# Performance work log

Measured on AMD Instinct MI355X. Metric: run time of the kernel, lower is better.

The kernel has to match this reference:

```python
import jax, jax.numpy as jnp
import numpy as np

KH, KW, PAD, G = 3, 3, 1, 4  # kernel, padding, deformable groups


def _bilinear_gather(xg, py, px):
    """xg: [B,G,C,Hin,Win]; py,px: [B,G,K,H,W] sample coords.
    Returns [B,G,C,K,H,W] with zero padding outside the image (mmcv semantics)."""
    B, Gd, C, Hin, Win = xg.shape
    y0 = jnp.floor(py)
    x0 = jnp.floor(px)
    wy1 = py - y0
    wx1 = px - x0
    wy0 = 1.0 - wy1
    wx0 = 1.0 - wx1
    xf = xg.reshape(B, Gd, C, Hin * Win)

    def gather(yi, xi):
        valid = (yi >= 0) & (yi < Hin) & (xi >= 0) & (xi < Win)
        yc = jnp.clip(yi, 0, Hin - 1).astype(jnp.int32)
        xc = jnp.clip(xi, 0, Win - 1).astype(jnp.int32)
        lin = (yc * Win + xc).reshape(B, Gd, 1, -1)  # [B,G,1,K*H*W]
        v = jnp.take_along_axis(xf, lin, axis=3).reshape(B, Gd, C, *yi.shape[2:])
        return v * valid[:, :, None].astype(xg.dtype)

    return (gather(y0, x0) * (wy0 * wx0)[:, :, None]
            + gather(y0, x0 + 1) * (wy0 * wx1)[:, :, None]
            + gather(y0 + 1, x0) * (wy1 * wx0)[:, :, None]
            + gather(y0 + 1, x0 + 1) * (wy1 * wx1)[:, :, None])


def setup_inputs() -> dict:
    key = jax.random.key(0)
    k1, k2, k3, k4 = jax.random.split(key, 4)
    B, Cin, Cout, H, W = 8, 256, 256, 64, 64
    x = jax.random.normal(k1, (B, Cin, H, W), dtype=jnp.float32)
    shape = jax.random.normal(k2, (B, 4, H, W), dtype=jnp.float32)
    # conv_offset: 1x1 conv, 4 -> G*2*KH*KW = 72 channels, no bias
    w_offset = jax.random.normal(k3, (G * 2 * KH * KW, 4), dtype=jnp.float32) * 0.1
    # conv_adaption: deform conv weight, no bias
    w_deform = jax.random.normal(k4, (Cout, Cin, KH, KW), dtype=jnp.float32) * 0.01
    return {"x": x, "shape": shape, "w_offset": w_offset, "w_deform": w_deform}


def reference(x, shape, w_offset, w_deform):
    B, Cin, H, W = x.shape
    Cout = w_deform.shape[0]
    K = KH * KW
    # 1x1 offset-predicting conv on detached shape
    shape = jax.lax.stop_gradient(shape)
    offset = jnp.einsum('oc,bchw->bohw', w_offset, shape)  # [B, G*2*K, H, W]
    off = offset.reshape(B, G, K, 2, H, W)  # mmcv layout: (dy, dx) per tap
    dy, dx = off[:, :, :, 0], off[:, :, :, 1]  # [B,G,K,H,W]
    # base sampling grid for each kernel tap
    ky, kx = jnp.meshgrid(jnp.arange(KH), jnp.arange(KW), indexing='ij')
    ky = ky.reshape(-1)
    kx = kx.reshape(-1)
    base_y = (ky - PAD)[:, None, None] + jnp.arange(H)[None, :, None]  # [K,H,1]
    base_x = (kx - PAD)[:, None, None] + jnp.arange(W)[None, None, :]  # [K,1,W]
    py = base_y[None, None].astype(x.dtype) + dy  # [B,G,K,H,W]
    px = base_x[None, None].astype(x.dtype) + dx
    xg = x.reshape(B, G, Cin // G, H, W)
    sampled = _bilinear_gather(xg, py, px)  # [B,G,Cpg,K,H,W]
    wr = w_deform.reshape(Cout, G, Cin // G, K)
    out = jnp.einsum('ogck,bgckhw->bohw', wr, sampled)
    return jax.nn.relu(out)
```

## Files before the change

### kernel.cpp

```cpp
#include <hip/hip_runtime.h>
#include <hip/hip_bf16.h>


#define Bn   8
#define CIN  256
#define COUT 256
#define Hn   64
#define Wn   64
#define Gn   4
#define Kn   9
#define CPG  64
#define GK   36

typedef float    f32x4 __attribute__((ext_vector_type(4)));
typedef _Float16 f16x2 __attribute__((ext_vector_type(2)));
typedef _Float16 f16x8 __attribute__((ext_vector_type(8)));

#define SWPAD 1156
#define HWT   32
__global__ void fa_prep(const float* __restrict__ x, const float* __restrict__ w,
                        _Float16* __restrict__ xt, _Float16* __restrict__ wfrag) {
    const int bid = blockIdx.x, t = threadIdx.x;
    __shared__ __align__(16) _Float16 spool[16 * SWPAD];
    if (bid < 1024) {
        _Float16* sT = spool;
        const int b = bid >> 7, tile = bid & 127;
        const int hw0 = tile * HWT;
        const int s = t >> 3, hwq = t & 7;
#pragma unroll
        for (int it = 0; it < 8; it++) {
            int c = it * 32 + s;
            float4 v = *(const float4*)(x + (((size_t)(b * CIN + c)) << 12) + hw0 + hwq * 4);
            const float* vf = (const float*)&v;
#pragma unroll
            for (int j = 0; j < 4; j++) {
                int hw = hwq * 4 + j;
                sT[hw * 256 + (c ^ (hwq << 3))] = (_Float16)vf[j];
            }
        }
        __syncthreads();
        const int cg = t & 31, hwr = t >> 5;
#pragma unroll
        for (int it = 0; it < 4; it++) {
            int hw = it * 8 + hwr;
            int q = hw >> 2;
            f16x8 v = *(const f16x8*)&sT[hw * 256 + ((cg ^ q) << 3)];
            *(f16x8*)&xt[(((size_t)b << 12) + hw0 + hw) * 256 + cg * 8] = v;
        }
    } else {
        _Float16* sw = spool;
        const int mt = (bid - 1024) >> 1, gh = (bid - 1024) & 1;
        const int o0 = mt * 16, g0 = gh * 2;
        const int r = t >> 4, tr = t & 15;
        const float* wp = w + (size_t)(o0 + r) * (CIN * Kn) + g0 * (CPG * Kn);
#pragma unroll
        for (int it = 0; it < 18; it++) {
            int off = it * 64 + tr * 4;
            float4 v = *(const float4*)(wp + off);
            _Float16* d = &sw[r * SWPAD + off];
            d[0] = (_Float16)v.x; d[1] = (_Float16)v.y;
            d[2] = (_Float16)v.z; d[3] = (_Float16)v.w;
        }
        __syncthreads();
#pragma unroll
        for (int it = 0; it < 9; it++) {
            int chunk = it * 256 + t;
            int lane = chunk & 63, ks = (chunk >> 6) & 1, gkl = chunk >> 7;
            int gl = gkl / Kn, k = gkl - gl * Kn;
            int gk = g0 * Kn + gkl;
            int ol = lane & 15;
            int cbase = ks * 32 + (lane >> 4) * 8;
            f16x8 v;
#pragma unroll
            for (int j = 0; j < 8; j++)
                v[j] = sw[ol * SWPAD + (gl * CPG + cbase + j) * Kn + k];
            *(f16x8*)&wfrag[(((size_t)gk * 16 + mt) * 2 + ks) * 512 + lane * 8] = v;
        }
    }
}

__global__ __launch_bounds__(512, 4)
void fa_main(const _Float16* __restrict__ xt, const float* __restrict__ shp,
             const float* __restrict__ w_off, const _Float16* __restrict__ wfrag,
             float* __restrict__ out) {
    const int blk = blockIdx.x;
    const int bp = blk >> 7, h = (blk >> 1) & 63, wh = blk & 1;
    const int w0 = wh * 32;
    const int t = threadIdx.x;
    const int wid = t >> 6, lane = t & 63;
    const int col = lane & 15, quad = lane >> 4;
    const int cg = t & 7, nl = (t >> 3) & 63;

    __shared__ __align__(16) int4 s_meta[GK * 64];
    __shared__ __align__(16) _Float16 sB[2][64 * 64];
    __shared__ float s_shp[2 * 4 * 32];
    __shared__ float s_woff[GK * 8];

    if (t < 256) {
        int bb = t >> 7, c = (t >> 5) & 3, wl = t & 31;
        s_shp[t] = shp[(((bp * 2 + bb) * 4 + c) << 12) + h * Wn + w0 + wl];
    }
    for (int u = t; u < GK * 8; u += 512) s_woff[u] = w_off[u];
    __syncthreads();

    for (int i = t; i < GK * 64; i += 512) {
        int gk = i >> 6, n = i & 63;
        int bb = n >> 5, wl = n & 31;
        int g = gk / Kn, k = gk - g * Kn;
        int ky = k / 3, kx = k - ky * 3;
        float dy = 0.f, dx = 0.f;
#pragma unroll
        for (int c = 0; c < 4; c++) {
            float sv = s_shp[(bb * 4 + c) * 32 + wl];
            dy = fmaf(s_woff[gk * 8 + c],     sv, dy);
            dx = fmaf(s_woff[gk * 8 + 4 + c], sv, dx);
        }
        float py = (float)(h + ky - 1) + dy;
        float px = (float)(w0 + wl + kx - 1) + dx;
        float y0 = floorf(py), x0 = floorf(px);
        float fy = py - y0, fx = px - x0;
        int iy = (int)y0, ix = (int)x0;
        bool y0v = (unsigned)iy       < (unsigned)Hn;
        bool y1v = (unsigned)(iy + 1) < (unsigned)Hn;
        bool x0v = (unsigned)ix       < (unsigned)Wn;
        bool x1v = (unsigned)(ix + 1) < (unsigned)Wn;
        int yc0 = min(max(iy, 0), Hn - 1), yc1 = min(max(iy + 1, 0), Hn - 1);
        int xc0 = min(max(ix, 0), Wn - 1), xc1 = min(max(ix + 1, 0), Wn - 1);
        int l00 = yc0 * Wn + xc0, l01 = yc0 * Wn + xc1;
        int l10 = yc1 * Wn + xc0, l11 = yc1 * Wn + xc1;
        float wy1 = fy, wy0 = 1.f - fy, wx1 = fx, wx0 = 1.f - fx;
        float w00 = (y0v && x0v) ? wy0 * wx0 : 0.f;
        float w01 = (y0v && x1v) ? wy0 * wx1 : 0.f;
        float w10 = (y1v && x0v) ? wy1 * wx0 : 0.f;
        float w11 = (y1v && x1v) ? wy1 * wx1 : 0.f;
        f16x2 p0, p1;
        p0.x = (_Float16)w00; p0.y = (_Float16)w01;
        p1.x = (_Float16)w10; p1.y = (_Float16)w11;
        s_meta[i] = make_int4(l00 | (l01 << 16), l10 | (l11 << 16),
                              __builtin_bit_cast(int, p0),
                              __builtin_bit_cast(int, p1));
    }

    f16x8 c4[4];
    int2  amv;
    const unsigned nBase = ((unsigned)(bp * 2 + (nl >> 5)) << 20) + (unsigned)cg * 8u;

    auto issue = [&](int gk) {
        int4 mv = s_meta[gk * 64 + nl];
        amv.x = mv.z; amv.y = mv.w;
        unsigned g = (unsigned)gk / (unsigned)Kn;
        unsigned base = nBase + g * 64u;
        c4[0] = *(const f16x8*)(xt + base + (((unsigned)mv.x & 0xffffu) << 8));
        c4[1] = *(const f16x8*)(xt + base + (((unsigned)mv.x >> 16)     << 8));
        c4[2] = *(const f16x8*)(xt + base + (((unsigned)mv.y & 0xffffu) << 8));
        c4[3] = *(const f16x8*)(xt + base + (((unsigned)mv.y >> 16)     << 8));
    };
    auto commit = [&](int buf) {
        f16x2 wv0 = __builtin_bit_cast(f16x2, amv.x);
        f16x2 wv1 = __builtin_bit_cast(f16x2, amv.y);
        f16x2 w00 = __builtin_shufflevector(wv0, wv0, 0, 0);
        f16x2 w01 = __builtin_shufflevector(wv0, wv0, 1, 1);
        f16x2 w10 = __builtin_shufflevector(wv1, wv1, 0, 0);
        f16x2 w11 = __builtin_shufflevector(wv1, wv1, 1, 1);
        const f16x2* a0p = (const f16x2*)&c4[0];
        const f16x2* a1p = (const f16x2*)&c4[1];
        const f16x2* a2p = (const f16x2*)&c4[2];
        const f16x2* a3p = (const f16x2*)&c4[3];
        f16x8 r;
        f16x2* rp = (f16x2*)&r;
#pragma unroll
        for (int p = 0; p < 4; p++) {
            f16x2 rv = w00 * a0p[p] + w01 * a1p[p]
                     + w10 * a2p[p] + w11 * a3p[p];
            rp[p] = rv;
        }
        *(f16x8*)&sB[buf][(nl * 8 + (cg ^ (nl & 7))) * 8] = r;
    };

    f32x4 acc[2][4];
#pragma unroll
    for (int mt = 0; mt < 2; mt++)
#pragma unroll
        for (int nt = 0; nt < 4; nt++) acc[mt][nt] = (f32x4){0.f, 0.f, 0.f, 0.f};

    __syncthreads();

    issue(0);
    commit(0);
    issue(1);
    __syncthreads();

    for (int gk = 0; gk < GK; gk++) {
        const int buf = gk & 1;
        const _Float16* wbase = wfrag + (((size_t)gk * 16 + wid * 2) * 2) * 512;
        f16x8 af[2][2];
#pragma unroll
        for (int ks = 0; ks < 2; ks++)
#pragma unroll
            for (int mt = 0; mt < 2; mt++)
                af[ks][mt] = *(const f16x8*)(wbase + ((size_t)(mt * 2 + ks) * 64 + lane) * 8);
        f16x8 bfv[2][4];
#pragma unroll
        for (int ks = 0; ks < 2; ks++)
#pragma unroll
            for (int nt = 0; nt < 4; nt++) {
                int n = nt * 16 + col;
                int cq8 = ks * 4 + quad;
                bfv[ks][nt] = *(const f16x8*)&sB[buf][(n * 8 + (cq8 ^ (n & 7))) * 8];
            }
        if (gk + 1 < GK) commit(buf ^ 1);
        if (gk + 2 < GK) issue(gk + 2);
#pragma unroll
        for (int ks = 0; ks < 2; ks++)
#pragma unroll
            for (int mt = 0; mt < 2; mt++)
#pragma unroll
                for (int nt = 0; nt < 4; nt++)
                    acc[mt][nt] = __builtin_amdgcn_mfma_f32_16x16x32_f16(
                        af[ks][mt], bfv[ks][nt], acc[mt][nt], 0, 0, 0);
        __syncthreads();
    }

#pragma unroll
    for (int mt = 0; mt < 2; mt++)
#pragma unroll
        for (int r = 0; r < 4; r++) {
            int o = wid * 32 + mt * 16 + quad * 4 + r;
#pragma unroll
            for (int nt = 0; nt < 4; nt++) {
                int n = nt * 16 + col;
                int b = bp * 2 + (n >> 5);
                int w = w0 + (n & 31);
                out[(((size_t)(b * COUT + o)) << 12) + h * Wn + w] =
                    fmaxf(acc[mt][nt][r], 0.f);
            }
        }
}

extern "C" void kernel_launch(void* const* d_in, const int* in_sizes, int n_in,
                              void* d_out, int out_size, void* d_ws, size_t ws_size,
                              hipStream_t stream) {
    const float* x     = (const float*)d_in[0];
    const float* shp   = (const float*)d_in[1];
    const float* w_off = (const float*)d_in[2];
    const float* w_def = (const float*)d_in[3];
    float* out = (float*)d_out;
    _Float16* wfrag = (_Float16*)d_ws;
    _Float16* xt    = (_Float16*)((char*)d_ws + (2u << 20));

    fa_prep<<<1024 + 32, 256, 0, stream>>>(x, w_def, xt, wfrag);
    fa_main<<<512, 512, 0, stream>>>(xt, shp, w_off, wfrag, out);
}
```

Baseline: 139.9 us.

## Halve per-block pixel tile to one batch row segment and double grid

Each block now covers 32 output pixels from a single batch image instead of 64 pixels spanning two images, so the grid grows from 512 to 1024 blocks. The gather is redistributed to 16 threads per pixel, each loading 4 halfs, and the MFMA N-tile shrinks from 4 to 2. Launch bounds now request 8 blocks per CU to raise occupancy and hide gather latency. The trade-off is that each block reloads the same weight fragments for half as much work, which doubles weight traffic per output and lowers MFMA reuse.

```diff
diff --git a/kernel.cpp b/kernel.cpp
--- a/kernel.cpp
+++ b/kernel.cpp
@@ -14,6 +14,7 @@
 
 typedef float    f32x4 __attribute__((ext_vector_type(4)));
 typedef _Float16 f16x2 __attribute__((ext_vector_type(2)));
+typedef _Float16 f16x4 __attribute__((ext_vector_type(4)));
 typedef _Float16 f16x8 __attribute__((ext_vector_type(8)));
 
 #define SWPAD 1156
@@ -79,39 +80,38 @@
     }
 }
 
-__global__ __launch_bounds__(512, 4)
+__global__ __launch_bounds__(512, 8)
 void fa_main(const _Float16* __restrict__ xt, const float* __restrict__ shp,
              const float* __restrict__ w_off, const _Float16* __restrict__ wfrag,
              float* __restrict__ out) {
     const int blk = blockIdx.x;
-    const int bp = blk >> 7, h = (blk >> 1) & 63, wh = blk & 1;
+    const int b = blk >> 7, h = (blk >> 1) & 63, wh = blk & 1;
     const int w0 = wh * 32;
     const int t = threadIdx.x;
     const int wid = t >> 6, lane = t & 63;
     const int col = lane & 15, quad = lane >> 4;
-    const int cg = t & 7, nl = (t >> 3) & 63;
-
-    __shared__ __align__(16) int4 s_meta[GK * 64];
-    __shared__ __align__(16) _Float16 sB[2][64 * 64];
-    __shared__ float s_shp[2 * 4 * 32];
+    const int cg = t & 15, nl = (t >> 4) & 31;
+
+    __shared__ __align__(16) int4 s_meta[GK * 32];
+    __shared__ __align__(16) _Float16 sB[2][32 * 64];
+    __shared__ float s_shp[4 * 32];
     __shared__ float s_woff[GK * 8];
 
-    if (t < 256) {
-        int bb = t >> 7, c = (t >> 5) & 3, wl = t & 31;
-        s_shp[t] = shp[(((bp * 2 + bb) * 4 + c) << 12) + h * Wn + w0 + wl];
+    if (t < 128) {
+        int c = t >> 5, wl = t & 31;
+        s_shp[t] = shp[(((b * 4 + c)) << 12) + h * Wn + w0 + wl];
     }
     for (int u = t; u < GK * 8; u += 512) s_woff[u] = w_off[u];
     __syncthreads();
 
-    for (int i = t; i < GK * 64; i += 512) {
-        int gk = i >> 6, n = i & 63;
-        int bb = n >> 5, wl = n & 31;
+    for (int i = t; i < GK * 32; i += 512) {
+        int gk = i >> 5, wl = i & 31;
         int g = gk / Kn, k = gk - g * Kn;
         int ky = k / 3, kx = k - ky * 3;
         float dy = 0.f, dx = 0.f;
 #pragma unroll
         for (int c = 0; c < 4; c++) {
-            float sv = s_shp[(bb * 4 + c) * 32 + wl];
+            float sv = s_shp[c * 32 + wl];
             dy = fmaf(s_woff[gk * 8 + c],     sv, dy);
             dx = fmaf(s_woff[gk * 8 + 4 + c], sv, dx);
         }
@@ -141,19 +141,19 @@
                               __builtin_bit_cast(int, p1));
     }
 
-    f16x8 c4[4];
+    f16x4 c4[4];
     int2  amv;
-    const unsigned nBase = ((unsigned)(bp * 2 + (nl >> 5)) << 20) + (unsigned)cg * 8u;
+    const unsigned nBase = ((unsigned)b << 20) + (unsigned)cg * 4u;
 
     auto issue = [&](int gk) {
-        int4 mv = s_meta[gk * 64 + nl];
+        int4 mv = s_meta[gk * 32 + nl];
         amv.x = mv.z; amv.y = mv.w;
         unsigned g = (unsigned)gk / (unsigned)Kn;
         unsigned base = nBase + g * 64u;
-        c4[0] = *(const f16x8*)(xt + base + (((unsigned)mv.x & 0xffffu) << 8));
-        c4[1] = *(const f16x8*)(xt + base + (((unsigned)mv.x >> 16)     << 8));
-        c4[2] = *(const f16x8*)(xt + base + (((unsigned)mv.y & 0xffffu) << 8));
-        c4[3] = *(const f16x8*)(xt + base + (((unsigned)mv.y >> 16)     << 8));
+        c4[0] = *(const f16x4*)(xt + base + (((unsigned)mv.x & 0xffffu) << 8));
+        c4[1] = *(const f16x4*)(xt + base + (((unsigned)mv.x >> 16)     << 8));
+        c4[2] = *(const f16x4*)(xt + base + (((unsigned)mv.y & 0xffffu) << 8));
+        c4[3] = *(const f16x4*)(xt + base + (((unsigned)mv.y >> 16)     << 8));
     };
     auto commit = [&](int buf) {
         f16x2 wv0 = __builtin_bit_cast(f16x2, amv.x);
@@ -166,22 +166,22 @@
         const f16x2* a1p = (const f16x2*)&c4[1];
         const f16x2* a2p = (const f16x2*)&c4[2];
         const f16x2* a3p = (const f16x2*)&c4[3];
-        f16x8 r;
+        f16x4 r;
         f16x2* rp = (f16x2*)&r;
 #pragma unroll
-        for (int p = 0; p < 4; p++) {
+        for (int p = 0; p < 2; p++) {
             f16x2 rv = w00 * a0p[p] + w01 * a1p[p]
                      + w10 * a2p[p] + w11 * a3p[p];
             rp[p] = rv;
         }
-        *(f16x8*)&sB[buf][(nl * 8 + (cg ^ (nl & 7))) * 8] = r;
+        *(f16x4*)&sB[buf][nl * 64 + (((cg >> 1) ^ (nl & 7)) << 3) + (cg & 1) * 4] = r;
     };
 
-    f32x4 acc[2][4];
+    f32x4 acc[2][2];
 #pragma unroll
     for (int mt = 0; mt < 2; mt++)
 #pragma unroll
-        for (int nt = 0; nt < 4; nt++) acc[mt][nt] = (f32x4){0.f, 0.f, 0.f, 0.f};
+        for (int nt = 0; nt < 2; nt++) acc[mt][nt] = (f32x4){0.f, 0.f, 0.f, 0.f};
 
     __syncthreads();
 
@@ -199,25 +199,24 @@
 #pragma unroll
             for (int mt = 0; mt < 2; mt++)
                 af[ks][mt] = *(const f16x8*)(wbase + ((size_t)(mt * 2 + ks) * 64 + lane) * 8);
-        f16x8 bfv[2][4];
-#pragma unroll
-        for (int ks = 0; ks < 2; ks++)
-#pragma unroll
-            for (int nt = 0; nt < 4; nt++) {
+        if (gk + 1 < GK) commit(buf ^ 1);
+        if (gk + 2 < GK) issue(gk + 2);
+#pragma unroll
+        for (int ks = 0; ks < 2; ks++) {
+            f16x8 bfv[2];
+#pragma unroll
+            for (int nt = 0; nt < 2; nt++) {
                 int n = nt * 16 + col;
                 int cq8 = ks * 4 + quad;
-                bfv[ks][nt] = *(const f16x8*)&sB[buf][(n * 8 + (cq8 ^ (n & 7))) * 8];
+                bfv[nt] = *(const f16x8*)&sB[buf][(n * 8 + (cq8 ^ (n & 7))) * 8];
             }
-        if (gk + 1 < GK) commit(buf ^ 1);
-        if (gk + 2 < GK) issue(gk + 2);
-#pragma unroll
-        for (int ks = 0; ks < 2; ks++)
 #pragma unroll
             for (int mt = 0; mt < 2; mt++)
 #pragma unroll
-                for (int nt = 0; nt < 4; nt++)
+                for (int nt = 0; nt < 2; nt++)
                     acc[mt][nt] = __builtin_amdgcn_mfma_f32_16x16x32_f16(
-                        af[ks][mt], bfv[ks][nt], acc[mt][nt], 0, 0, 0);
+                        af[ks][mt], bfv[nt], acc[mt][nt], 0, 0, 0);
+        }
         __syncthreads();
     }
 
@@ -227,11 +226,9 @@
         for (int r = 0; r < 4; r++) {
             int o = wid * 32 + mt * 16 + quad * 4 + r;
 #pragma unroll
-            for (int nt = 0; nt < 4; nt++) {
+            for (int nt = 0; nt < 2; nt++) {
                 int n = nt * 16 + col;
-                int b = bp * 2 + (n >> 5);
-                int w = w0 + (n & 31);
-                out[(((size_t)(b * COUT + o)) << 12) + h * Wn + w] =
+                out[(((size_t)(b * COUT + o)) << 12) + h * Wn + w0 + n] =
                     fmaxf(acc[mt][nt][r], 0.f);
             }
         }
@@ -249,5 +246,5 @@
     _Float16* xt    = (_Float16*)((char*)d_ws + (2u << 20));
 
     fa_prep<<<1024 + 32, 256, 0, stream>>>(x, w_def, xt, wfrag);
-    fa_main<<<512, 512, 0, stream>>>(xt, shp, w_off, wfrag, out);
+    fa_main<<<1024, 512, 0, stream>>>(xt, shp, w_off, wfrag, out);
 }
```

Result: slower. 165.3 us (+18.2%).
